# Optimization experiments

Hardware: AMD Instinct MI355X
Metric: run time of the kernel (lower is better)

Reference implementation:

```python
import jax, jax.numpy as jnp
import numpy as np

ORDER = 63
CODEBOOK_SIZE = 256
MIN_DATA = 1
N_ITER = 5
EPS = 1e-05
PERTURB = 1e-05


def setup_inputs() -> dict:
    key = jax.random.key(0)
    x = jax.random.normal(key, (131072, ORDER + 1), dtype=jnp.float32)
    return {"x": x}


def _e_step(x, cb, T):
    # squared euclidean distances via gram trick: (T, curr)
    d2 = jnp.sum(x * x, 1)[:, None] - 2.0 * (x @ cb.T) + jnp.sum(cb * cb, 1)[None, :]
    idx = jnp.argmin(d2, axis=1)
    xq = cb[idx]
    dist = jnp.sum((x - xq) ** 2) / T
    return idx, dist


def _m_step(x, idx, curr, key):
    D = x.shape[1]
    ones = jnp.ones((x.shape[0],), x.dtype)
    n_data = jax.ops.segment_sum(ones, idx, num_segments=curr)        # histc
    mask = n_data >= MIN_DATA
    sums = jax.ops.segment_sum(x, idx, num_segments=curr)             # scatter_add
    cent = sums / jnp.maximum(n_data, 1.0)[:, None]
    m = jnp.argmax(n_data)
    r = jax.random.normal(key, (curr, D), x.dtype) * PERTURB
    nm = (~mask).astype(x.dtype)
    # empty clusters reseeded from the largest cluster, perturbed
    new = jnp.where(mask[:, None], cent, cent[m][None, :] - r)
    cnt = jnp.sum(nm)
    corr = jnp.sum(r * nm[:, None], axis=0) / jnp.maximum(cnt, 1.0)
    new = new.at[m].add(jnp.where(cnt > 0, corr, jnp.zeros_like(corr)))
    return new


def _lbg(x):
    T, D = x.shape
    K = CODEBOOK_SIZE
    codebook = jnp.full((K, D), 1e10, x.dtype).at[0].set(jnp.mean(x, axis=0))
    distance = jnp.asarray(jnp.inf, x.dtype)
    base = jax.random.key(42)
    curr = 1
    split = 0
    while curr * 2 <= K:  # static loop over log2(K) binary splits
        key_s = jax.random.fold_in(base, split)
        kr, kloop = jax.random.split(key_s)
        r = jax.random.normal(kr, (curr, D), x.dtype) * PERTURB
        codebook = codebook.at[curr:2 * curr].set(codebook[:curr] - r).at[:curr].add(r)
        curr *= 2
        prev = distance

        def body(carry, n, curr=curr):
            cb, prev_d, dist, done, key = carry
            idx, d_new = _e_step(x, cb, T)
            change = jnp.abs(prev_d - d_new)
            conv = (n > 0) & (change / (d_new + 1e-16) < EPS)
            key, sub = jax.random.split(key)
            cb_new = _m_step(x, idx, curr, sub)
            stop = done | conv
            cb_out = jnp.where(stop, cb, cb_new)        # skip m-step on convergence/break
            dist_out = jnp.where(done, dist, d_new)     # distance assigned before break
            prev_out = jnp.where(stop, prev_d, d_new)
            return (cb_out, prev_out, dist_out, stop, key), None

        carry0 = (codebook[:curr], prev, distance, jnp.asarray(False), kloop)
        (cb_fin, _, distance, _, _), _ = jax.lax.scan(body, carry0, jnp.arange(N_ITER))
        codebook = codebook.at[:curr].set(cb_fin)
        split += 1
    return codebook, distance


def reference(x):
    return _lbg(x)
```

## Files before the change

kernel.cpp:

```cpp
#include <hip/hip_runtime.h>
#include <stdint.h>


#define NPTS 131072
#define DIMS 64
#define KCB  256
#define NCB  16

struct LbgState { float dist; float prev; unsigned int done; unsigned int k0, k1; unsigned int pad; };

__device__ __forceinline__ uint32_t rotl32(uint32_t v, int n){ return (v<<n)|(v>>(32-n)); }

__device__ __forceinline__ void tf2x32(uint32_t k0, uint32_t k1, uint32_t x0, uint32_t x1,
                                       uint32_t& o0, uint32_t& o1){
  uint32_t ks2 = k0 ^ k1 ^ 0x1BD11BDAu;
  x0 += k0; x1 += k1;
  #define TFR(r) { x0 += x1; x1 = rotl32(x1, r); x1 ^= x0; }
  TFR(13) TFR(15) TFR(26) TFR(6)
  x0 += k1; x1 += ks2 + 1u;
  TFR(17) TFR(29) TFR(16) TFR(24)
  x0 += ks2; x1 += k0 + 2u;
  TFR(13) TFR(15) TFR(26) TFR(6)
  x0 += k0; x1 += k1 + 3u;
  TFR(17) TFR(29) TFR(16) TFR(24)
  x0 += k1; x1 += ks2 + 4u;
  TFR(13) TFR(15) TFR(26) TFR(6)
  x0 += ks2; x1 += k0 + 5u;
  #undef TFR
  o0 = x0; o1 = x1;
}

__device__ __forceinline__ float xla_erfinv_f32(float x){
  float w = -log1pf(-x*x);
  float p;
  if (w < 5.0f){
    w = w - 2.5f;
    p = 2.81022636e-08f;
    p = fmaf(p, w, 3.43273939e-07f);
    p = fmaf(p, w, -3.5233877e-06f);
    p = fmaf(p, w, -4.39150654e-06f);
    p = fmaf(p, w, 0.00021858087f);
    p = fmaf(p, w, -0.00125372503f);
    p = fmaf(p, w, -0.00417768164f);
    p = fmaf(p, w, 0.246640727f);
    p = fmaf(p, w, 1.50140941f);
  } else {
    w = sqrtf(w) - 3.0f;
    p = -0.000200214257f;
    p = fmaf(p, w, 0.000100950558f);
    p = fmaf(p, w, 0.00134934322f);
    p = fmaf(p, w, -0.00367342844f);
    p = fmaf(p, w, 0.00573950773f);
    p = fmaf(p, w, -0.0076224613f);
    p = fmaf(p, w, 0.00943887047f);
    p = fmaf(p, w, 1.00167406f);
    p = fmaf(p, w, 2.83297682f);
  }
  return p * x;
}

__device__ __forceinline__ float jax_normal_elem(uint32_t k0, uint32_t k1, uint32_t j){
  uint32_t o0, o1; tf2x32(k0, k1, 0u, j, o0, o1);
  uint32_t bits = o0 ^ o1;
  uint32_t fb = (bits >> 9) | 0x3f800000u;
  float f = __uint_as_float(fb) - 1.0f;
  const float lo = -0.99999994f;
  float u = f * 2.0f + lo;
  u = fmaxf(lo, u);
  return 1.41421356f * xla_erfinv_f32(u);
}

__device__ void do_split(float* __restrict__ cb, float* __restrict__ cnorm,
                         unsigned long long* __restrict__ sums,
                         unsigned int* __restrict__ ndata,
                         unsigned long long* __restrict__ distacc,
                         LbgState* __restrict__ st, int curr, int split, int t){
  __shared__ uint32_t kr0s, kr1s;
  if (t == 0){
    uint32_t ks0, ks1, a0, a1, b0, b1;
    tf2x32(0u, 42u, 0u, (uint32_t)split, ks0, ks1);
    tf2x32(ks0, ks1, 0u, 0u, a0, a1);
    tf2x32(ks0, ks1, 0u, 1u, b0, b1);
    kr0s = a0; kr1s = a1;
    st->k0 = b0; st->k1 = b1;
    st->prev = st->dist;
    st->done = 0u;
  }
  __syncthreads();
  const int n = curr * DIMS;
  for (int e = t; e < n; e += 256){
    int c = e >> 6, d = e & 63;
    float rv = jax_normal_elem(kr0s, kr1s, (uint32_t)e) * 1e-5f;
    float old = cb[c*DIMS + d];
    cb[(curr + c)*DIMS + d] = old - rv;
    cb[c*DIMS + d]          = old + rv;
  }
  __syncthreads();
  const int c2 = curr * 2;
  for (int c = t; c < c2; c += 256){
    float s = 0.f;
    for (int d = 0; d < DIMS; d++){ float vv = cb[c*DIMS+d]; s += vv*vv; }
    cnorm[c] = s;
  }
  for (int e = t; e < c2*DIMS; e += 256) sums[e] = 0ull;
  for (int c = t; c < c2; c += 256) ndata[c] = 0u;
  if (t == 0) *distacc = 0ull;
}

__global__ void mean_kernel(const float* __restrict__ x, unsigned long long* __restrict__ macc,
                            float* __restrict__ cb, float* __restrict__ cnorm,
                            unsigned long long* __restrict__ sums,
                            unsigned int* __restrict__ ndata,
                            unsigned long long* __restrict__ distacc,
                            LbgState* __restrict__ st, unsigned int* __restrict__ mcnt){
  __shared__ double part[256];
  __shared__ float stage[16*64];
  __shared__ int islast;
  const int t = threadIdx.x;
  const int d = t & 63;
  const int w = t >> 6;
  const size_t base = (size_t)blockIdx.x * 1024;
  const int lrow = t >> 4;
  const int lcol = (t & 15) * 4;

  const float4* xg = reinterpret_cast<const float4*>(x);
  float4 nxt = xg[((base + lrow) * DIMS + lcol) >> 2];
  double s = 0.0;
  for (int tt = 0; tt < 64; tt++){
    float4 cur = nxt;
    if (tt < 63)
      nxt = xg[((base + (tt+1)*16 + lrow) * DIMS + lcol) >> 2];
    __syncthreads();
    *reinterpret_cast<float4*>(&stage[lrow*DIMS + lcol]) = cur;
    __syncthreads();
    s += (double)stage[(w    )*DIMS + d];
    s += (double)stage[(w + 4)*DIMS + d];
    s += (double)stage[(w + 8)*DIMS + d];
    s += (double)stage[(w +12)*DIMS + d];
  }
  part[t] = s;
  __syncthreads();
  if (t < 64){
    double tot = part[t] + part[64+t] + part[128+t] + part[192+t];
    atomicAdd(&macc[t], (unsigned long long)__double2ll_rn(tot * 1099511627776.0));
  }
  __threadfence();
  __syncthreads();
  if (t == 0) islast = (atomicAdd(mcnt, 1u) == (unsigned)(gridDim.x - 1));
  __syncthreads();
  if (!islast) return;

  if (t < 64){
    long long mv = (long long)atomicAdd(&macc[t], 0ull);
    double mean = (double)mv * (1.0/1099511627776.0) / 131072.0;
    cb[t] = (float)mean;
  }
  for (int e = t; e < KCB*DIMS; e += 256)
    if (e >= 64) cb[e] = 1e10f;
  if (t == 0){
    st->dist = __builtin_inff();
    st->prev = __builtin_inff();
    st->done = 0u;
    atomicExch(mcnt, 0u);
  }
  __syncthreads();
  do_split(cb, cnorm, sums, ndata, distacc, st, 1, 0, t);
}

template<int CURR>
__global__ __launch_bounds__(256, 4)
void estep_kernel(const float* __restrict__ x, const float* __restrict__ cb,
                  const float* __restrict__ cnorm, unsigned char* __restrict__ bidx8,
                  unsigned long long* __restrict__ distacc, const LbgState* __restrict__ st){
  if (st->done) return;
  const int t = threadIdx.x;
  const int lane = t & 63;
  const int p = blockIdx.x * 256 + t;

  float xv[DIMS];
  const float4* xp = reinterpret_cast<const float4*>(x + (size_t)p * DIMS);
  #pragma unroll
  for (int i = 0; i < 16; i++){
    float4 v = xp[i];
    xv[4*i+0] = v.x; xv[4*i+1] = v.y; xv[4*i+2] = v.z; xv[4*i+3] = v.w;
  }
  float xx = 0.f;
  #pragma unroll
  for (int d = 0; d < DIMS; d++) xx += xv[d] * xv[d];

  constexpr int NJ = (CURR < 4) ? CURR : 4;
  float best = __builtin_inff();
  int bi = 0;
  for (int j0 = 0; j0 < CURR; j0 += NJ){
    const float* crow = cb + (size_t)j0 * DIMS;
    float acc[NJ];
    #pragma unroll
    for (int k = 0; k < NJ; k++) acc[k] = 0.f;
    #pragma unroll
    for (int d = 0; d < DIMS; d++){
      #pragma unroll
      for (int k = 0; k < NJ; k++)
        acc[k] = fmaf(xv[d], crow[k*DIMS + d], acc[k]);
    }
    #pragma unroll
    for (int k = 0; k < NJ; k++){
      float d2 = (xx - 2.0f*acc[k]) + cnorm[j0 + k];
      if (d2 < best){ best = d2; bi = j0 + k; }
    }
  }
  bidx8[p] = (unsigned char)bi;

  double dd = 0.0;
  const float4* cbv = reinterpret_cast<const float4*>(cb + (size_t)bi * DIMS);
  #pragma unroll
  for (int i = 0; i < 16; i++){
    float4 b = cbv[i];
    float df, sq;
    df = xv[4*i+0] - b.x; sq = df*df; dd += (double)sq;
    df = xv[4*i+1] - b.y; sq = df*df; dd += (double)sq;
    df = xv[4*i+2] - b.z; sq = df*df; dd += (double)sq;
    df = xv[4*i+3] - b.w; sq = df*df; dd += (double)sq;
  }
  for (int off = 32; off > 0; off >>= 1) dd += __shfl_down(dd, off);
  if (lane == 0)
    atomicAdd(distacc, (unsigned long long)__double2ll_rn(dd * 4294967296.0));
}

template<int CURR>
__global__ __launch_bounds__(256, 4)
void estep_sw(const float* __restrict__ x, const float* __restrict__ cb,
              const float* __restrict__ cnorm, unsigned char* __restrict__ bidx8,
              unsigned long long* __restrict__ distacc, const LbgState* __restrict__ st){
  if (st->done) return;
  constexpr int CPW = CURR / 4;
  constexpr int NJG = (CPW < 16) ? CPW : 16;
  constexpr int NG = CPW / NJG;
  __shared__ float4 xs[16*128];
  __shared__ float sxx[128];
  __shared__ float sbest[4*128];
  __shared__ int   sidx [4*128];
  const int t = threadIdx.x;
  const int lane = t & 63;
  const int w = __builtin_amdgcn_readfirstlane(t >> 6);
  const int pbase = blockIdx.x * 128;

  {
    const int p = t & 127, h = t >> 7;
    const float4* xg = reinterpret_cast<const float4*>(x) + (size_t)(pbase + p) * 16 + h * 8;
    #pragma unroll
    for (int j = 0; j < 8; j++)
      xs[(h*8 + j)*128 + p] = xg[j];
  }
  __syncthreads();
  if (t < 128){
    float xx = 0.f;
    #pragma unroll
    for (int k4 = 0; k4 < 16; k4++){
      float4 v = xs[k4*128 + t];
      xx = fmaf(v.x, v.x, xx); xx = fmaf(v.y, v.y, xx);
      xx = fmaf(v.z, v.z, xx); xx = fmaf(v.w, v.w, xx);
    }
    sxx[t] = xx;
  }
  __syncthreads();

  const float xx0 = sxx[lane];
  const float xx1 = sxx[64 + lane];
  float best0 = __builtin_inff(), best1 = __builtin_inff();
  int bi0 = 0, bi1 = 0;
  const float4* cbg = reinterpret_cast<const float4*>(cb);
  const int cwbase = w * CPW;

  for (int g = 0; g < NG; g++){
    const int c0 = cwbase + g*NJG;
    float acc0[NJG], acc1[NJG];
    #pragma unroll
    for (int cj = 0; cj < NJG; cj++){ acc0[cj] = 0.f; acc1[cj] = 0.f; }
    for (int k4 = 0; k4 < 16; k4++){
      float4 xf0 = xs[k4*128 + lane];
      float4 xf1 = xs[k4*128 + 64 + lane];
      #pragma unroll
      for (int cj = 0; cj < NJG; cj++){
        float4 cf = cbg[(size_t)(c0 + cj)*16 + k4];
        acc0[cj] = fmaf(xf0.x, cf.x, acc0[cj]);
        acc0[cj] = fmaf(xf0.y, cf.y, acc0[cj]);
        acc0[cj] = fmaf(xf0.z, cf.z, acc0[cj]);
        acc0[cj] = fmaf(xf0.w, cf.w, acc0[cj]);
        acc1[cj] = fmaf(xf1.x, cf.x, acc1[cj]);
        acc1[cj] = fmaf(xf1.y, cf.y, acc1[cj]);
        acc1[cj] = fmaf(xf1.z, cf.z, acc1[cj]);
        acc1[cj] = fmaf(xf1.w, cf.w, acc1[cj]);
      }
    }
    #pragma unroll
    for (int cj = 0; cj < NJG; cj++){
      float cn = cnorm[c0 + cj];
      float d20 = (xx0 - 2.0f*acc0[cj]) + cn;
      if (d20 < best0){ best0 = d20; bi0 = c0 + cj; }
      float d21 = (xx1 - 2.0f*acc1[cj]) + cn;
      if (d21 < best1){ best1 = d21; bi1 = c0 + cj; }
    }
  }
  sbest[w*128 + lane]      = best0;  sidx[w*128 + lane]      = bi0;
  sbest[w*128 + 64 + lane] = best1;  sidx[w*128 + 64 + lane] = bi1;
  __syncthreads();

  if (t < 128){
    float best = sbest[t];
    int bi = sidx[t];
    #pragma unroll
    for (int ww = 1; ww < 4; ww++){
      float ob = sbest[ww*128 + t];
      int   oi = sidx [ww*128 + t];
      if (ob < best){ best = ob; bi = oi; }
    }
    bidx8[pbase + t] = (unsigned char)bi;
    const float4* cbv = cbg + (size_t)bi * 16;
    double dd = 0.0;
    #pragma unroll
    for (int k4 = 0; k4 < 16; k4++){
      float4 xv = xs[k4*128 + t];
      float4 b = cbv[k4];
      float df, sq;
      df = xv.x - b.x; sq = df*df; dd += (double)sq;
      df = xv.y - b.y; sq = df*df; dd += (double)sq;
      df = xv.z - b.z; sq = df*df; dd += (double)sq;
      df = xv.w - b.w; sq = df*df; dd += (double)sq;
    }
    for (int off = 32; off > 0; off >>= 1) dd += __shfl_down(dd, off);
    if ((t & 63) == 0)
      atomicAdd(distacc, (unsigned long long)__double2ll_rn(dd * 4294967296.0));
  }
}

template<int CURR, int NBLK>
__global__ __launch_bounds__(256)
void gather_kernel(const float* __restrict__ x, const unsigned char* __restrict__ bidx8,
                   unsigned long long* __restrict__ sums, unsigned int* __restrict__ ndata,
                   const LbgState* __restrict__ st){
  if (st->done) return;
  constexpr int CLOG = __builtin_ctz(CURR);
  constexpr int NCHUNK = NBLK / CURR;
  constexpr int PPC = NPTS / NCHUNK;
  constexpr int NPW = PPC / 4;
  __shared__ long long sacc[4][64][4];
  __shared__ unsigned int scw[4];
  const int t = threadIdx.x;
  const int lane = t & 63;
  const int w = t >> 6;
  const int c = blockIdx.x & (CURR - 1);
  const int chunk = blockIdx.x >> CLOG;
  const int pbase = chunk * PPC + w * NPW;
  const int sub = lane >> 4;
  const int dof = (lane & 15) * 4;

  long long a0 = 0, a1 = 0, a2 = 0, a3 = 0;
  unsigned int cnt = 0;
  int q0=0,q1=0,q2=0,q3=0,q4=0,q5=0,q6=0,q7=0, qn=0;
  const uint32_t* bp = reinterpret_cast<const uint32_t*>(bidx8 + pbase);
  for (int i = 0; i < NPW; i += 256){
    const uint32_t b4 = bp[(i >> 2) + lane];
    #pragma unroll
    for (int s = 0; s < 4; s++){
      unsigned long long m = __ballot(((b4 >> (8*s)) & 255u) == (unsigned)c);
      cnt += (unsigned int)__popcll(m);
      while (m){
        const int bit = __builtin_ctzll(m);
        m &= m - 1ull;
        const int p = pbase + i + bit*4 + s;
        if      (qn == 0) q0 = p;
        else if (qn == 1) q1 = p;
        else if (qn == 2) q2 = p;
        else if (qn == 3) q3 = p;
        else if (qn == 4) q4 = p;
        else if (qn == 5) q5 = p;
        else if (qn == 6) q6 = p;
        else              q7 = p;
        qn++;
        if (qn == 8){
          const int rA = (sub==0)?q0:(sub==1)?q1:(sub==2)?q2:q3;
          const int rB = (sub==0)?q4:(sub==1)?q5:(sub==2)?q6:q7;
          const float4 vA = *reinterpret_cast<const float4*>(x + (size_t)rA * DIMS + dof);
          const float4 vB = *reinterpret_cast<const float4*>(x + (size_t)rB * DIMS + dof);
          a0 += (long long)__double2int_rn((double)vA.x * 1048576.0);
          a1 += (long long)__double2int_rn((double)vA.y * 1048576.0);
          a2 += (long long)__double2int_rn((double)vA.z * 1048576.0);
          a3 += (long long)__double2int_rn((double)vA.w * 1048576.0);
          a0 += (long long)__double2int_rn((double)vB.x * 1048576.0);
          a1 += (long long)__double2int_rn((double)vB.y * 1048576.0);
          a2 += (long long)__double2int_rn((double)vB.z * 1048576.0);
          a3 += (long long)__double2int_rn((double)vB.w * 1048576.0);
          qn = 0;
        }
      }
    }
  }
  if (qn > 0){
    const int i1 = (qn > 1) ? q1 : q0;
    const int i2 = (qn > 2) ? q2 : q0;
    const int i3 = (qn > 3) ? q3 : q0;
    const int i4 = (qn > 4) ? q4 : q0;
    const int i5 = (qn > 5) ? q5 : q0;
    const int i6 = (qn > 6) ? q6 : q0;
    const int rA = (sub==0)?q0:(sub==1)?i1:(sub==2)?i2:i3;
    const int rB = (sub==0)?i4:(sub==1)?i5:(sub==2)?i6:q0;
    const float4 vA = *reinterpret_cast<const float4*>(x + (size_t)rA * DIMS + dof);
    const float4 vB = *reinterpret_cast<const float4*>(x + (size_t)rB * DIMS + dof);
    if (sub < qn){
      a0 += (long long)__double2int_rn((double)vA.x * 1048576.0);
      a1 += (long long)__double2int_rn((double)vA.y * 1048576.0);
      a2 += (long long)__double2int_rn((double)vA.z * 1048576.0);
      a3 += (long long)__double2int_rn((double)vA.w * 1048576.0);
    }
    if (sub + 4 < qn){
      a0 += (long long)__double2int_rn((double)vB.x * 1048576.0);
      a1 += (long long)__double2int_rn((double)vB.y * 1048576.0);
      a2 += (long long)__double2int_rn((double)vB.z * 1048576.0);
      a3 += (long long)__double2int_rn((double)vB.w * 1048576.0);
    }
  }
  sacc[w][lane][0] = a0; sacc[w][lane][1] = a1;
  sacc[w][lane][2] = a2; sacc[w][lane][3] = a3;
  if (lane == 0) scw[w] = cnt;
  __syncthreads();
  if (w == 0){
    long long tot = 0;
    #pragma unroll
    for (int ww = 0; ww < 4; ww++)
      #pragma unroll
      for (int r = 0; r < 4; r++)
        tot += sacc[ww][r*16 + (lane >> 2)][lane & 3];
    if (tot) atomicAdd(&sums[c*DIMS + lane], (unsigned long long)(tot * 1048576ll));
    if (lane == 0){
      unsigned int ct = scw[0] + scw[1] + scw[2] + scw[3];
      if (ct) atomicAdd(&ndata[c], ct);
    }
  }
}

__global__ void control_kernel(float* __restrict__ cb, float* __restrict__ cnorm,
                               const unsigned long long* __restrict__ sums_in,
                               unsigned long long* __restrict__ sums_out,
                               const unsigned int* __restrict__ ndata_in,
                               unsigned int* __restrict__ ndata_out,
                               const unsigned long long* __restrict__ distacc_in,
                               unsigned long long* __restrict__ distacc_out,
                               const LbgState* __restrict__ st_in,
                               LbgState* __restrict__ st_out,
                               int curr, int n_iter, int next_split){
  __shared__ float cm[64];
  __shared__ int redv[256];
  __shared__ int redi[256];
  __shared__ int s_m, s_cnt;
  const int t = threadIdx.x;
  const int b = blockIdx.x;

  const unsigned int done0 = st_in->done;
  float d_new = 0.f;
  int stop = 1;
  uint32_t sub0 = 0, sub1 = 0, nk0 = 0, nk1 = 0;
  if (!done0){
    double ddv = (double)(long long)(*distacc_in) * (1.0/4294967296.0);
    float sf = (float)ddv;
    d_new = sf / 131072.0f;
    float change = fabsf(st_in->prev - d_new);
    int conv = (n_iter > 0) && (change / (d_new + 1e-16f) < 1e-5f);
    stop = conv;
    if (!conv){
      tf2x32(st_in->k0, st_in->k1, 0u, 0u, nk0, nk1);
      tf2x32(st_in->k0, st_in->k1, 0u, 1u, sub0, sub1);
    }
  }

  const int rpb = (curr + NCB - 1) / NCB;
  const int r0 = b * rpb;
  int r1 = r0 + rpb; if (r1 > curr) r1 = curr;

  if (!done0 && !stop){
    int v = (t < curr) ? (int)ndata_in[t] : -1;
    redv[t] = v; redi[t] = t;
    __syncthreads();
    for (int s = 128; s > 0; s >>= 1){
      if (t < s){
        if (redv[t+s] > redv[t] || (redv[t+s] == redv[t] && redi[t+s] < redi[t])){
          redv[t] = redv[t+s]; redi[t] = redi[t+s];
        }
      }
      __syncthreads();
    }
    if (t == 0) s_m = redi[0];
    __syncthreads();
    redv[t] = (t < curr && ndata_in[t] == 0u) ? 1 : 0;
    __syncthreads();
    for (int s = 128; s > 0; s >>= 1){
      if (t < s) redv[t] += redv[t+s];
      __syncthreads();
    }
    if (t == 0) s_cnt = redv[0];
    __syncthreads();
    const int m = s_m;
    const int cntE = s_cnt;

    if (t < 64){
      unsigned int nm_ = ndata_in[m]; if (nm_ < 1u) nm_ = 1u;
      double cd = (double)(long long)sums_in[m*DIMS + t] * (1.0/1099511627776.0) / (double)nm_;
      cm[t] = (float)cd;
    }
    __syncthreads();

    for (int e = r0*DIMS + t; e < r1*DIMS; e += 256){
      int cc = e >> 6, d = e & 63;
      if (cc == m) continue;
      float nv;
      unsigned int nd = ndata_in[cc];
      if (nd >= 1u){
        double cd = (double)(long long)sums_in[e] * (1.0/1099511627776.0) / (double)nd;
        nv = (float)cd;
      } else {
        float rv = jax_normal_elem(sub0, sub1, (uint32_t)e) * 1e-5f;
        nv = cm[d] - rv;
      }
      cb[e] = nv;
    }
    if (m >= r0 && m < r1 && t < 64){
      float add = 0.f;
      if (cntE > 0){
        float acc = 0.f;
        for (int cc = 0; cc < curr; cc++){
          if (ndata_in[cc] == 0u)
            acc += jax_normal_elem(sub0, sub1, (uint32_t)(cc*DIMS + t)) * 1e-5f;
        }
        add = acc / fmaxf((float)cntE, 1.0f);
      }
      cb[m*DIMS + t] = cm[t] + add;
    }
    __syncthreads();

    for (int cc = r0 + t; cc < r1; cc += 256){
      float s = 0.f;
      for (int d = 0; d < DIMS; d++){ float vv = cb[cc*DIMS+d]; s += vv*vv; }
      cnorm[cc] = s;
    }
  }

  const int rows_next = (n_iter == 4 && curr < KCB) ? 2*curr : curr;
  for (int e = b*256 + t; e < rows_next*DIMS; e += NCB*256) sums_out[e] = 0ull;
  for (int cc = b*256 + t; cc < rows_next; cc += NCB*256) ndata_out[cc] = 0u;
  if (b == 0 && t == 0) *distacc_out = 0ull;

  if (b == 0 && t == 0){
    const float fin_dist = done0 ? st_in->dist : d_new;
    LbgState ns;
    ns.dist = fin_dist;
    if (done0 || stop){
      ns.prev = st_in->prev; ns.done = 1u; ns.k0 = st_in->k0; ns.k1 = st_in->k1;
    } else {
      ns.prev = d_new; ns.done = 0u; ns.k0 = nk0; ns.k1 = nk1;
    }
    ns.pad = 0u;
    if (n_iter == 4){
      if (curr < KCB){
        uint32_t ks0, ks1, sa0, sa1, sb0, sb1;
        tf2x32(0u, 42u, 0u, (uint32_t)next_split, ks0, ks1);
        tf2x32(ks0, ks1, 0u, 0u, sa0, sa1);
        tf2x32(ks0, ks1, 0u, 1u, sb0, sb1);
        ns.k0 = sb0; ns.k1 = sb1;
        ns.prev = fin_dist;
        ns.done = 0u;
      } else {
        cb[KCB*DIMS] = fin_dist;
      }
    }
    *st_out = ns;
  }

  if (n_iter == 4 && curr < KCB){
    uint32_t ks0, ks1, kr0, kr1;
    tf2x32(0u, 42u, 0u, (uint32_t)next_split, ks0, ks1);
    tf2x32(ks0, ks1, 0u, 0u, kr0, kr1);
    __syncthreads();
    for (int e = r0*DIMS + t; e < r1*DIMS; e += 256){
      int cc = e >> 6, d = e & 63;
      float rv = jax_normal_elem(kr0, kr1, (uint32_t)e) * 1e-5f;
      float old = cb[e];
      cb[(curr + cc)*DIMS + d] = old - rv;
      cb[e]                    = old + rv;
    }
    __syncthreads();
    for (int cc = r0 + t; cc < r1; cc += 256){
      float s0 = 0.f, s1 = 0.f;
      for (int d = 0; d < DIMS; d++){
        float v0 = cb[cc*DIMS + d];        s0 += v0*v0;
        float v1 = cb[(curr+cc)*DIMS + d]; s1 += v1*v1;
      }
      cnorm[cc] = s0;
      cnorm[curr + cc] = s1;
    }
  }
}

extern "C" void kernel_launch(void* const* d_in, const int* in_sizes, int n_in,
                              void* d_out, int out_size, void* d_ws, size_t ws_size,
                              hipStream_t stream){
  const float* x = (const float*)d_in[0];
  float* cb = (float*)d_out;
  char* ws = (char*)d_ws;
  unsigned long long* sums0   = (unsigned long long*)(ws + 0);
  unsigned long long* sums1   = (unsigned long long*)(ws + 131072);
  unsigned long long* macc    = (unsigned long long*)(ws + 262144);
  unsigned long long* dist0   = (unsigned long long*)(ws + 262656);
  unsigned long long* dist1   = (unsigned long long*)(ws + 262664);
  LbgState* st0               = (LbgState*)(ws + 262672);
  LbgState* st1               = (LbgState*)(ws + 262704);
  unsigned int* nd0           = (unsigned int*)(ws + 262736);
  unsigned int* nd1           = (unsigned int*)(ws + 263760);
  float* cnorm                = (float*)(ws + 264784);
  unsigned char* bidx8        = (unsigned char*)(ws + 265808);
  unsigned int* mcnt          = (unsigned int*)(ws + 396880);

  unsigned long long* sums[2] = { sums0, sums1 };
  unsigned long long* dac[2]  = { dist0, dist1 };
  LbgState* st[2]             = { st0, st1 };
  unsigned int* nd[2]         = { nd0, nd1 };

  hipMemsetAsync(d_ws, 0, 396884, stream);
  mean_kernel<<<128, 256, 0, stream>>>(x, macc, cb, cnorm, sums0, nd0, dist0, st0, mcnt);

  int g = 0;
  for (int split = 0; split < 8; split++){
    const int curr = 2 << split;
    for (int n = 0; n < 5; n++){
      const int pi = g & 1, po = pi ^ 1;
      switch (curr){
        case 2:   estep_kernel<2>  <<<512,256,0,stream>>>(x,cb,cnorm,bidx8,dac[pi],st[pi]);
                  gather_kernel<2,256>   <<<256, 256,0,stream>>>(x,bidx8,sums[pi],nd[pi],st[pi]); break;
        case 4:   estep_kernel<4>  <<<512,256,0,stream>>>(x,cb,cnorm,bidx8,dac[pi],st[pi]);
                  gather_kernel<4,512>   <<<512, 256,0,stream>>>(x,bidx8,sums[pi],nd[pi],st[pi]); break;
        case 8:   estep_sw<8>    <<<1024,256,0,stream>>>(x,cb,cnorm,bidx8,dac[pi],st[pi]);
                  gather_kernel<8,1024>  <<<1024,256,0,stream>>>(x,bidx8,sums[pi],nd[pi],st[pi]); break;
        case 16:  estep_sw<16>   <<<1024,256,0,stream>>>(x,cb,cnorm,bidx8,dac[pi],st[pi]);
                  gather_kernel<16,2048> <<<2048,256,0,stream>>>(x,bidx8,sums[pi],nd[pi],st[pi]); break;
        case 32:  estep_sw<32>   <<<1024,256,0,stream>>>(x,cb,cnorm,bidx8,dac[pi],st[pi]);
                  gather_kernel<32,2048> <<<2048,256,0,stream>>>(x,bidx8,sums[pi],nd[pi],st[pi]); break;
        case 64:  estep_sw<64>   <<<1024,256,0,stream>>>(x,cb,cnorm,bidx8,dac[pi],st[pi]);
                  gather_kernel<64,2048> <<<2048,256,0,stream>>>(x,bidx8,sums[pi],nd[pi],st[pi]); break;
        case 128: estep_sw<128>  <<<1024,256,0,stream>>>(x,cb,cnorm,bidx8,dac[pi],st[pi]);
                  gather_kernel<128,2048><<<2048,256,0,stream>>>(x,bidx8,sums[pi],nd[pi],st[pi]); break;
        case 256: estep_sw<256>  <<<1024,256,0,stream>>>(x,cb,cnorm,bidx8,dac[pi],st[pi]);
                  gather_kernel<256,2048><<<2048,256,0,stream>>>(x,bidx8,sums[pi],nd[pi],st[pi]); break;
      }
      control_kernel<<<NCB, 256, 0, stream>>>(cb, cnorm,
          sums[pi], sums[po], nd[pi], nd[po], dac[pi], dac[po],
          st[pi], st[po], curr, n, split+1);
      g++;
    }
  }
}
```

Measured before the change: 2.743 ms.

## Hold point vectors in registers across codeword loop in E-step kernel

The E-step kernel now loads each thread's two 64-dim points from shared memory into registers once, computes their squared norms in registers, and loops over codewords in groups of 4. Before, it re-read the points from LDS for every group of up to 16 codewords and used a separate norm pass with an extra barrier. This removes repeated LDS traffic and one sync, but holds 128 floats per thread in registers, so launch bounds are lowered from 4 to 3 blocks per CU. The risks are lower occupancy and register spilling.

```diff
diff --git a/kernel.cpp b/kernel.cpp
--- a/kernel.cpp
+++ b/kernel.cpp
@@ -227,16 +227,14 @@
 }
 
 template<int CURR>
-__global__ __launch_bounds__(256, 4)
-void estep_sw(const float* __restrict__ x, const float* __restrict__ cb,
+__global__ __launch_bounds__(256, 3)
+void estep_rx(const float* __restrict__ x, const float* __restrict__ cb,
               const float* __restrict__ cnorm, unsigned char* __restrict__ bidx8,
               unsigned long long* __restrict__ distacc, const LbgState* __restrict__ st){
   if (st->done) return;
   constexpr int CPW = CURR / 4;
-  constexpr int NJG = (CPW < 16) ? CPW : 16;
-  constexpr int NG = CPW / NJG;
+  constexpr int UNR = (CPW >= 4) ? 4 : CPW;
   __shared__ float4 xs[16*128];
-  __shared__ float sxx[128];
   __shared__ float sbest[4*128];
   __shared__ int   sidx [4*128];
   const int t = threadIdx.x;
@@ -252,53 +250,49 @@
       xs[(h*8 + j)*128 + p] = xg[j];
   }
   __syncthreads();
-  if (t < 128){
-    float xx = 0.f;
-    #pragma unroll
-    for (int k4 = 0; k4 < 16; k4++){
-      float4 v = xs[k4*128 + t];
-      xx = fmaf(v.x, v.x, xx); xx = fmaf(v.y, v.y, xx);
-      xx = fmaf(v.z, v.z, xx); xx = fmaf(v.w, v.w, xx);
-    }
-    sxx[t] = xx;
-  }
-  __syncthreads();
-
-  const float xx0 = sxx[lane];
-  const float xx1 = sxx[64 + lane];
+
+  float4 xa[16], xb[16];
+  #pragma unroll
+  for (int i = 0; i < 16; i++){
+    xa[i] = xs[i*128 + lane];
+    xb[i] = xs[i*128 + 64 + lane];
+  }
+  float xx0 = 0.f, xx1 = 0.f;
+  #pragma unroll
+  for (int i = 0; i < 16; i++){
+    xx0 = fmaf(xa[i].x, xa[i].x, xx0); xx0 = fmaf(xa[i].y, xa[i].y, xx0);
+    xx0 = fmaf(xa[i].z, xa[i].z, xx0); xx0 = fmaf(xa[i].w, xa[i].w, xx0);
+    xx1 = fmaf(xb[i].x, xb[i].x, xx1); xx1 = fmaf(xb[i].y, xb[i].y, xx1);
+    xx1 = fmaf(xb[i].z, xb[i].z, xx1); xx1 = fmaf(xb[i].w, xb[i].w, xx1);
+  }
+
   float best0 = __builtin_inff(), best1 = __builtin_inff();
   int bi0 = 0, bi1 = 0;
   const float4* cbg = reinterpret_cast<const float4*>(cb);
   const int cwbase = w * CPW;
 
-  for (int g = 0; g < NG; g++){
-    const int c0 = cwbase + g*NJG;
-    float acc0[NJG], acc1[NJG];
-    #pragma unroll
-    for (int cj = 0; cj < NJG; cj++){ acc0[cj] = 0.f; acc1[cj] = 0.f; }
-    for (int k4 = 0; k4 < 16; k4++){
-      float4 xf0 = xs[k4*128 + lane];
-      float4 xf1 = xs[k4*128 + 64 + lane];
+  for (int cj = 0; cj < CPW; cj += UNR){
+    float a0[UNR], a1[UNR];
+    #pragma unroll
+    for (int u = 0; u < UNR; u++){ a0[u] = 0.f; a1[u] = 0.f; }
+    #pragma unroll
+    for (int i = 0; i < 16; i++){
       #pragma unroll
-      for (int cj = 0; cj < NJG; cj++){
-        float4 cf = cbg[(size_t)(c0 + cj)*16 + k4];
-        acc0[cj] = fmaf(xf0.x, cf.x, acc0[cj]);
-        acc0[cj] = fmaf(xf0.y, cf.y, acc0[cj]);
-        acc0[cj] = fmaf(xf0.z, cf.z, acc0[cj]);
-        acc0[cj] = fmaf(xf0.w, cf.w, acc0[cj]);
-        acc1[cj] = fmaf(xf1.x, cf.x, acc1[cj]);
-        acc1[cj] = fmaf(xf1.y, cf.y, acc1[cj]);
-        acc1[cj] = fmaf(xf1.z, cf.z, acc1[cj]);
-        acc1[cj] = fmaf(xf1.w, cf.w, acc1[cj]);
-      }
-    }
-    #pragma unroll
-    for (int cj = 0; cj < NJG; cj++){
-      float cn = cnorm[c0 + cj];
-      float d20 = (xx0 - 2.0f*acc0[cj]) + cn;
-      if (d20 < best0){ best0 = d20; bi0 = c0 + cj; }
-      float d21 = (xx1 - 2.0f*acc1[cj]) + cn;
-      if (d21 < best1){ best1 = d21; bi1 = c0 + cj; }
+      for (int u = 0; u < UNR; u++){
+        float4 cf = cbg[(size_t)(cwbase + cj + u)*16 + i];
+        a0[u] = fmaf(xa[i].x, cf.x, a0[u]); a0[u] = fmaf(xa[i].y, cf.y, a0[u]);
+        a0[u] = fmaf(xa[i].z, cf.z, a0[u]); a0[u] = fmaf(xa[i].w, cf.w, a0[u]);
+        a1[u] = fmaf(xb[i].x, cf.x, a1[u]); a1[u] = fmaf(xb[i].y, cf.y, a1[u]);
+        a1[u] = fmaf(xb[i].z, cf.z, a1[u]); a1[u] = fmaf(xb[i].w, cf.w, a1[u]);
+      }
+    }
+    #pragma unroll
+    for (int u = 0; u < UNR; u++){
+      float cn = cnorm[cwbase + cj + u];
+      float d20 = (xx0 - 2.0f*a0[u]) + cn;
+      if (d20 < best0){ best0 = d20; bi0 = cwbase + cj + u; }
+      float d21 = (xx1 - 2.0f*a1[u]) + cn;
+      if (d21 < best1){ best1 = d21; bi1 = cwbase + cj + u; }
     }
   }
   sbest[w*128 + lane]      = best0;  sidx[w*128 + lane]      = bi0;
@@ -318,9 +312,9 @@
     const float4* cbv = cbg + (size_t)bi * 16;
     double dd = 0.0;
     #pragma unroll
-    for (int k4 = 0; k4 < 16; k4++){
-      float4 xv = xs[k4*128 + t];
-      float4 b = cbv[k4];
+    for (int i = 0; i < 16; i++){
+      float4 xv = (w == 0) ? xa[i] : xb[i];
+      float4 b = cbv[i];
       float df, sq;
       df = xv.x - b.x; sq = df*df; dd += (double)sq;
       df = xv.y - b.y; sq = df*df; dd += (double)sq;
@@ -636,17 +630,17 @@
                   gather_kernel<2,256>   <<<256, 256,0,stream>>>(x,bidx8,sums[pi],nd[pi],st[pi]); break;
         case 4:   estep_kernel<4>  <<<512,256,0,stream>>>(x,cb,cnorm,bidx8,dac[pi],st[pi]);
                   gather_kernel<4,512>   <<<512, 256,0,stream>>>(x,bidx8,sums[pi],nd[pi],st[pi]); break;
-        case 8:   estep_sw<8>    <<<1024,256,0,stream>>>(x,cb,cnorm,bidx8,dac[pi],st[pi]);
+        case 8:   estep_rx<8>    <<<1024,256,0,stream>>>(x,cb,cnorm,bidx8,dac[pi],st[pi]);
                   gather_kernel<8,1024>  <<<1024,256,0,stream>>>(x,bidx8,sums[pi],nd[pi],st[pi]); break;
-        case 16:  estep_sw<16>   <<<1024,256,0,stream>>>(x,cb,cnorm,bidx8,dac[pi],st[pi]);
+        case 16:  estep_rx<16>   <<<1024,256,0,stream>>>(x,cb,cnorm,bidx8,dac[pi],st[pi]);
                   gather_kernel<16,2048> <<<2048,256,0,stream>>>(x,bidx8,sums[pi],nd[pi],st[pi]); break;
-        case 32:  estep_sw<32>   <<<1024,256,0,stream>>>(x,cb,cnorm,bidx8,dac[pi],st[pi]);
+        case 32:  estep_rx<32>   <<<1024,256,0,stream>>>(x,cb,cnorm,bidx8,dac[pi],st[pi]);
                   gather_kernel<32,2048> <<<2048,256,0,stream>>>(x,bidx8,sums[pi],nd[pi],st[pi]); break;
-        case 64:  estep_sw<64>   <<<1024,256,0,stream>>>(x,cb,cnorm,bidx8,dac[pi],st[pi]);
+        case 64:  estep_rx<64>   <<<1024,256,0,stream>>>(x,cb,cnorm,bidx8,dac[pi],st[pi]);
                   gather_kernel<64,2048> <<<2048,256,0,stream>>>(x,bidx8,sums[pi],nd[pi],st[pi]); break;
-        case 128: estep_sw<128>  <<<1024,256,0,stream>>>(x,cb,cnorm,bidx8,dac[pi],st[pi]);
+        case 128: estep_rx<128>  <<<1024,256,0,stream>>>(x,cb,cnorm,bidx8,dac[pi],st[pi]);
                   gather_kernel<128,2048><<<2048,256,0,stream>>>(x,bidx8,sums[pi],nd[pi],st[pi]); break;
-        case 256: estep_sw<256>  <<<1024,256,0,stream>>>(x,cb,cnorm,bidx8,dac[pi],st[pi]);
+        case 256: estep_rx<256>  <<<1024,256,0,stream>>>(x,cb,cnorm,bidx8,dac[pi],st[pi]);
                   gather_kernel<256,2048><<<2048,256,0,stream>>>(x,bidx8,sums[pi],nd[pi],st[pi]); break;
       }
       control_kernel<<<NCB, 256, 0, stream>>>(cb, cnorm,
```

New measurement: 3.497 ms. 27.5% more time.
